# Kernel optimization log

Hardware: AMD Instinct MI355X
Metric: run time of the kernel (lower is better)

Reference implementation:

```python
import jax, jax.numpy as jnp
import numpy as np

D_MODEL = 512
HEADS = 8
CTX = 2048
BATCH = 4
SEQ = 2048


def make_rotary_matrix(context_window, d):
    # Faithful to the source, including theta = 10000 ** (-2*(i-1)/d)
    i = np.arange(d // 2)
    theta = 10000.0 ** (-2.0 * (i - 1) / d)  # [d/2]
    pos = np.arange(context_window)
    m_theta = pos[:, None] * theta[None, :]  # [m, d/2]
    cos, sin = np.cos(m_theta), np.sin(m_theta)
    R = np.zeros((context_window, d, d), dtype=np.float32)
    even, odd = 2 * i, 2 * i + 1
    R[:, even, even] = cos
    R[:, even, odd] = -sin
    R[:, odd, even] = sin
    R[:, odd, odd] = cos
    return jnp.asarray(R)


def setup_inputs() -> dict:
    key = jax.random.key(0)
    ks = jax.random.split(key, 8)
    s = 1.0 / np.sqrt(D_MODEL)
    x = jax.random.normal(ks[0], (BATCH, SEQ, D_MODEL), dtype=jnp.float32)
    Wq = jax.random.normal(ks[1], (D_MODEL, D_MODEL), dtype=jnp.float32) * s
    Wk = jax.random.normal(ks[2], (D_MODEL, D_MODEL), dtype=jnp.float32) * s
    Wv = jax.random.normal(ks[3], (D_MODEL, D_MODEL), dtype=jnp.float32) * s
    in_proj_w = jax.random.normal(ks[4], (3 * D_MODEL, D_MODEL), dtype=jnp.float32) * s
    in_proj_b = jax.random.normal(ks[5], (3 * D_MODEL,), dtype=jnp.float32) * 0.01
    out_w = jax.random.normal(ks[6], (D_MODEL, D_MODEL), dtype=jnp.float32) * s
    out_b = jax.random.normal(ks[7], (D_MODEL,), dtype=jnp.float32) * 0.01
    R = make_rotary_matrix(CTX, D_MODEL)
    return {"x": x, "Wq": Wq, "Wk": Wk, "Wv": Wv, "R": R,
            "in_proj_w": in_proj_w, "in_proj_b": in_proj_b,
            "out_w": out_w, "out_b": out_b}


def reference(x, Wq, Wk, Wv, R, in_proj_w, in_proj_b, out_w, out_b):
    b, m, d = x.shape
    h = HEADS
    hd = d // h
    # outer QKV projections (bias=False)
    q = x @ Wq.T
    k = x @ Wk.T
    v = x @ Wv.T
    # dense per-position rotary rotation: q_out[b,p,:] = q[b,p,:] @ R[p]
    Rm = R[:m]
    q = jnp.einsum('bmd,mde->bme', q, Rm)
    k = jnp.einsum('bmd,mde->bme', k, Rm)
    v = jnp.einsum('bmd,mde->bme', v, Rm)
    # nn.MultiheadAttention in_proj (bias=True) -- dropout skipped (eval)
    wq_i, wk_i, wv_i = jnp.split(in_proj_w, 3, axis=0)
    bq, bk, bv = jnp.split(in_proj_b, 3, axis=0)
    qp = (q @ wq_i.T + bq).reshape(b, m, h, hd).transpose(0, 2, 1, 3)
    kp = (k @ wk_i.T + bk).reshape(b, m, h, hd).transpose(0, 2, 1, 3)
    vp = (v @ wv_i.T + bv).reshape(b, m, h, hd).transpose(0, 2, 1, 3)
    scale = 1.0 / np.sqrt(hd)
    scores = jnp.einsum('bhqd,bhkd->bhqk', qp, kp) * scale
    causal = jnp.triu(jnp.full((m, m), -jnp.inf, dtype=scores.dtype), k=1)
    attn = jax.nn.softmax(scores + causal, axis=-1)
    out = jnp.einsum('bhqk,bhkd->bhqd', attn, vp)
    out = out.transpose(0, 2, 1, 3).reshape(b, m, d)
    return out @ out_w.T + out_b
```

## Files before the change

### kernel.cpp

```cpp
#include <hip/hip_runtime.h>
#include <cmath>

typedef unsigned short u16;
typedef __bf16 bf16x8 __attribute__((ext_vector_type(8)));
typedef float f32x4 __attribute__((ext_vector_type(4)));

#define SEQL 2048
#define NH 8
#define HD 64

static __device__ __forceinline__ u16 f2bf(float f) {
  union { float f; unsigned u; } v; v.f = f;
  unsigned u = v.u;
  unsigned r = (u + 0x7FFFu + ((u >> 16) & 1u)) >> 16;
  return (u16)r;
}
static __device__ __forceinline__ float bf2f(u16 h) {
  union { unsigned u; float f; } v; v.u = ((unsigned)h) << 16;
  return v.f;
}

__global__ __launch_bounds__(256) void cvt_kernel(const float* __restrict__ in,
                                                  u16* __restrict__ out, int n) {
  int i = (blockIdx.x * 256 + threadIdx.x) * 4;
  if (i < n) {
    float4 f = *(const float4*)(in + i);
    ushort4 o;
    o.x = f2bf(f.x); o.y = f2bf(f.y); o.z = f2bf(f.z); o.w = f2bf(f.w);
    *(ushort4*)(out + i) = o;
  }
}

__global__ __launch_bounds__(256) void rot_table_kernel(float2* __restrict__ T) {
  int m = blockIdx.x, i = threadIdx.x;
  double theta = pow(10000.0, -2.0 * ((double)i - 1.0) / 512.0);
  double a = (double)m * theta;
  T[m * 256 + i] = make_float2((float)cos(a), (float)sin(a));
}

__global__ __launch_bounds__(256) void rope_kernel(u16* __restrict__ QKV,
                                                   const float2* __restrict__ T) {
  int row = blockIdx.x;
  int i = threadIdx.x;
  int m = row & 2047;
  float2 cs = T[m * 256 + i];
  float c = cs.x, s = cs.y;
  size_t base = (size_t)row * 1536 + 2 * i;
  #pragma unroll
  for (int seg = 0; seg < 3; ++seg) {
    u16* p = QKV + base + seg * 512;
    ushort2 eo = *(ushort2*)p;
    float e = bf2f(eo.x), o = bf2f(eo.y);
    ushort2 w;
    w.x = f2bf(e * c + o * s);
    w.y = f2bf(-e * s + o * c);
    *(ushort2*)p = w;
  }
}

template<int MODE>
__global__ __launch_bounds__(256) void gemm_bt(const u16* __restrict__ A, int lda,
                                               const u16* __restrict__ B, int ldb,
                                               const float* __restrict__ bias,
                                               void* __restrict__ Cv, int ldc) {
  __shared__ u16 As[128 * 80];
  __shared__ u16 Bs[128 * 80];
  int tid = threadIdx.x;
  int wid = tid >> 6, lane = tid & 63, quad = lane >> 4, l16 = lane & 15;
  int m0 = blockIdx.y * 128, n0 = blockIdx.x * 128;
  int wm = (wid >> 1) * 64, wn = (wid & 1) * 64;
  f32x4 acc[4][4] = {};
  for (int kb = 0; kb < 512; kb += 64) {
    #pragma unroll
    for (int s = 0; s < 4; ++s) {
      int slot = tid + s * 256;
      int row = slot >> 3, seg = slot & 7;
      *(uint4*)(&As[row * 80 + seg * 8]) =
          *(const uint4*)(A + (size_t)(m0 + row) * lda + kb + seg * 8);
      *(uint4*)(&Bs[row * 80 + seg * 8]) =
          *(const uint4*)(B + (size_t)(n0 + row) * ldb + kb + seg * 8);
    }
    __syncthreads();
    #pragma unroll
    for (int kk = 0; kk < 2; ++kk) {
      bf16x8 af[4], bfr[4];
      #pragma unroll
      for (int i = 0; i < 4; ++i)
        af[i] = *(const bf16x8*)(&As[(wm + 16 * i + l16) * 80 + quad * 8 + kk * 32]);
      #pragma unroll
      for (int j = 0; j < 4; ++j)
        bfr[j] = *(const bf16x8*)(&Bs[(wn + 16 * j + l16) * 80 + quad * 8 + kk * 32]);
      #pragma unroll
      for (int i = 0; i < 4; ++i)
        #pragma unroll
        for (int j = 0; j < 4; ++j)
          acc[i][j] = __builtin_amdgcn_mfma_f32_16x16x32_bf16(af[i], bfr[j], acc[i][j], 0, 0, 0);
    }
    __syncthreads();
  }
  #pragma unroll
  for (int i = 0; i < 4; ++i)
    #pragma unroll
    for (int j = 0; j < 4; ++j)
      #pragma unroll
      for (int r = 0; r < 4; ++r) {
        int row = m0 + wm + 16 * i + quad * 4 + r;
        int col = n0 + wn + 16 * j + l16;
        float v = acc[i][j][r];
        if (MODE >= 1) v += bias[col];
        if (MODE == 0) {
          ((u16*)Cv)[(size_t)row * ldc + col] = f2bf(v);
        } else if (MODE == 1) {
          int bb = row >> 11, mm = row & 2047;
          int h = col >> 6, dd = col & 63;
          ((u16*)Cv)[(((size_t)(bb * NH + h)) * SEQL + mm) * HD + dd] = f2bf(v);
        } else {
          ((float*)Cv)[(size_t)row * ldc + col] = v;
        }
      }
}

__global__ __launch_bounds__(256) void flash_kernel(const u16* __restrict__ Q,
                                                    const u16* __restrict__ K,
                                                    const u16* __restrict__ V,
                                                    u16* __restrict__ O) {
  __shared__ u16 Ks[64 * 80];
  __shared__ u16 Vt[64 * 80];
  __shared__ u16 Ps[4 * 16 * 80];
  int tid = threadIdx.x;
  int wid = tid >> 6, lane = tid & 63, quad = lane >> 4, l16 = lane & 15;
  int bh = blockIdx.y;
  int b = bh >> 3, h = bh & 7;
  int q0 = blockIdx.x * 64;
  const u16* Qb = Q + (size_t)bh * SEQL * HD;
  const u16* Kb = K + (size_t)bh * SEQL * HD;
  const u16* Vb = V + (size_t)bh * SEQL * HD;

  int qrow = q0 + wid * 16 + l16;
  bf16x8 qfrag0 = *(const bf16x8*)(Qb + (size_t)qrow * HD + quad * 8);
  bf16x8 qfrag1 = *(const bf16x8*)(Qb + (size_t)qrow * HD + quad * 8 + 32);

  f32x4 o_acc[4] = {};
  float m_i[4], l_i[4];
  #pragma unroll
  for (int r = 0; r < 4; ++r) { m_i[r] = -__builtin_inff(); l_i[r] = 0.f; }

  int nkb = q0 / 64 + 1;
  for (int kb = 0; kb < nkb; ++kb) {
    int k0 = kb * 64;
    #pragma unroll
    for (int s = 0; s < 2; ++s) {
      int slot = tid + s * 256;
      int row = slot >> 3, seg = slot & 7;
      uint4 kv = *(const uint4*)(Kb + (size_t)(k0 + row) * HD + seg * 8);
      *(uint4*)(&Ks[row * 80 + seg * 8]) = kv;
      union { uint4 v; u16 hx[8]; } tv;
      tv.v = *(const uint4*)(Vb + (size_t)(k0 + row) * HD + seg * 8);
      #pragma unroll
      for (int e = 0; e < 8; ++e) Vt[(seg * 8 + e) * 80 + row] = tv.hx[e];
    }
    __syncthreads();

    f32x4 s_acc[4] = {};
    #pragma unroll
    for (int j = 0; j < 4; ++j) {
      bf16x8 bk0 = *(const bf16x8*)(&Ks[(j * 16 + l16) * 80 + quad * 8]);
      bf16x8 bk1 = *(const bf16x8*)(&Ks[(j * 16 + l16) * 80 + quad * 8 + 32]);
      s_acc[j] = __builtin_amdgcn_mfma_f32_16x16x32_bf16(qfrag0, bk0, s_acc[j], 0, 0, 0);
      s_acc[j] = __builtin_amdgcn_mfma_f32_16x16x32_bf16(qfrag1, bk1, s_acc[j], 0, 0, 0);
    }
    bool diag = (k0 == q0);
    #pragma unroll
    for (int j = 0; j < 4; ++j)
      #pragma unroll
      for (int r = 0; r < 4; ++r) {
        float sv = s_acc[j][r] * 0.125f;
        if (diag) {
          int keyl = j * 16 + l16;
          int rowl = wid * 16 + quad * 4 + r;
          if (keyl > rowl) sv = -__builtin_inff();
        }
        s_acc[j][r] = sv;
      }
    float p[4][4], alpha[4];
    #pragma unroll
    for (int r = 0; r < 4; ++r) {
      float mx = fmaxf(fmaxf(s_acc[0][r], s_acc[1][r]), fmaxf(s_acc[2][r], s_acc[3][r]));
      #pragma unroll
      for (int off = 1; off < 16; off <<= 1) mx = fmaxf(mx, __shfl_xor(mx, off, 64));
      float m_new = fmaxf(m_i[r], mx);
      alpha[r] = __expf(m_i[r] - m_new);
      float rs = 0.f;
      #pragma unroll
      for (int j = 0; j < 4; ++j) { float pv = __expf(s_acc[j][r] - m_new); p[j][r] = pv; rs += pv; }
      #pragma unroll
      for (int off = 1; off < 16; off <<= 1) rs += __shfl_xor(rs, off, 64);
      l_i[r] = l_i[r] * alpha[r] + rs;
      m_i[r] = m_new;
    }
    #pragma unroll
    for (int j = 0; j < 4; ++j)
      #pragma unroll
      for (int r = 0; r < 4; ++r) o_acc[j][r] *= alpha[r];

    u16* Pw = &Ps[wid * 16 * 80];
    #pragma unroll
    for (int j = 0; j < 4; ++j)
      #pragma unroll
      for (int r = 0; r < 4; ++r)
        Pw[(quad * 4 + r) * 80 + j * 16 + l16] = f2bf(p[j][r]);
    bf16x8 pf0 = *(const bf16x8*)(&Pw[l16 * 80 + quad * 8]);
    bf16x8 pf1 = *(const bf16x8*)(&Pw[l16 * 80 + quad * 8 + 32]);
    #pragma unroll
    for (int j = 0; j < 4; ++j) {
      bf16x8 bv0 = *(const bf16x8*)(&Vt[(j * 16 + l16) * 80 + quad * 8]);
      bf16x8 bv1 = *(const bf16x8*)(&Vt[(j * 16 + l16) * 80 + quad * 8 + 32]);
      o_acc[j] = __builtin_amdgcn_mfma_f32_16x16x32_bf16(pf0, bv0, o_acc[j], 0, 0, 0);
      o_acc[j] = __builtin_amdgcn_mfma_f32_16x16x32_bf16(pf1, bv1, o_acc[j], 0, 0, 0);
    }
    __syncthreads();
  }
  #pragma unroll
  for (int j = 0; j < 4; ++j)
    #pragma unroll
    for (int r = 0; r < 4; ++r) {
      int m = q0 + wid * 16 + quad * 4 + r;
      float v = o_acc[j][r] / l_i[r];
      O[((size_t)(b * SEQL + m)) * 512 + h * HD + j * 16 + l16] = f2bf(v);
    }
}

extern "C" void kernel_launch(void* const* d_in, const int* in_sizes, int n_in,
                              void* d_out, int out_size, void* d_ws, size_t ws_size,
                              hipStream_t stream) {
  const float* x   = (const float*)d_in[0];
  const float* Wq  = (const float*)d_in[1];
  const float* Wk  = (const float*)d_in[2];
  const float* Wv  = (const float*)d_in[3];
  const float* ipw = (const float*)d_in[5];
  const float* ipb = (const float*)d_in[6];
  const float* ow  = (const float*)d_in[7];
  const float* ob  = (const float*)d_in[8];
  float* out = (float*)d_out;

  char* w = (char*)d_ws;
  auto alloc = [&](size_t bytes) { void* p = w; w += bytes; return p; };
  u16* xb    = (u16*)alloc(8192UL * 512 * 2);
  u16* Wcatb = (u16*)alloc(3UL * 512 * 512 * 2);
  u16* ipwb  = (u16*)alloc(1536UL * 512 * 2);
  u16* owb   = (u16*)alloc(512UL * 512 * 2);
  u16* QKV0  = (u16*)alloc(8192UL * 1536 * 2);
  u16* qp    = (u16*)alloc(8192UL * 512 * 2);
  u16* kp    = (u16*)alloc(8192UL * 512 * 2);
  u16* vp    = (u16*)alloc(8192UL * 512 * 2);
  u16* Ob    = (u16*)alloc(8192UL * 512 * 2);
  float2* T  = (float2*)alloc(2048UL * 256 * sizeof(float2));

  rot_table_kernel<<<2048, 256, 0, stream>>>(T);
  cvt_kernel<<<4194304 / 1024, 256, 0, stream>>>(x, xb, 4194304);
  cvt_kernel<<<262144 / 1024, 256, 0, stream>>>(Wq, Wcatb, 262144);
  cvt_kernel<<<262144 / 1024, 256, 0, stream>>>(Wk, Wcatb + 262144, 262144);
  cvt_kernel<<<262144 / 1024, 256, 0, stream>>>(Wv, Wcatb + 524288, 262144);
  cvt_kernel<<<786432 / 1024, 256, 0, stream>>>(ipw, ipwb, 786432);
  cvt_kernel<<<262144 / 1024, 256, 0, stream>>>(ow, owb, 262144);

  gemm_bt<0><<<dim3(12, 64), 256, 0, stream>>>(xb, 512, Wcatb, 512, nullptr, QKV0, 1536);
  rope_kernel<<<8192, 256, 0, stream>>>(QKV0, T);
  gemm_bt<1><<<dim3(4, 64), 256, 0, stream>>>(QKV0,        1536, ipwb,               512, ipb,        qp, 0);
  gemm_bt<1><<<dim3(4, 64), 256, 0, stream>>>(QKV0 + 512,  1536, ipwb + 512 * 512,   512, ipb + 512,  kp, 0);
  gemm_bt<1><<<dim3(4, 64), 256, 0, stream>>>(QKV0 + 1024, 1536, ipwb + 1024 * 512,  512, ipb + 1024, vp, 0);
  flash_kernel<<<dim3(32, 32), 256, 0, stream>>>(qp, kp, vp, Ob);
  gemm_bt<2><<<dim3(4, 64), 256, 0, stream>>>(Ob, 512, owb, 512, ob, out, 512);
}
```

Measured before the change: 2.531 ms.

## Merge in-proj GEMMs, pre-transpose V, and give each flash block two query tiles

The three per-segment in-projection GEMMs become one launch, which writes Q and K in head-major layout and V already transposed. The flash kernel now loads V tiles with vector copies instead of scalar LDS scatter-transposes. Each flash block processes 128 query rows as two 64-row tiles that share every K/V tile load, halving K/V traffic per query. The cost is fewer blocks (512), more registers per thread, and strided scalar stores for the transposed V in the GEMM epilogue.

```diff
diff --git a/kernel.cpp b/kernel.cpp
--- a/kernel.cpp
+++ b/kernel.cpp
@@ -8,6 +8,7 @@
 #define SEQL 2048
 #define NH 8
 #define HD 64
+#define MROWS 8192
 
 static __device__ __forceinline__ u16 f2bf(float f) {
   union { float f; unsigned u; } v; v.f = f;
@@ -74,11 +75,11 @@
     #pragma unroll
     for (int s = 0; s < 4; ++s) {
       int slot = tid + s * 256;
-      int row = slot >> 3, seg = slot & 7;
-      *(uint4*)(&As[row * 80 + seg * 8]) =
-          *(const uint4*)(A + (size_t)(m0 + row) * lda + kb + seg * 8);
-      *(uint4*)(&Bs[row * 80 + seg * 8]) =
-          *(const uint4*)(B + (size_t)(n0 + row) * ldb + kb + seg * 8);
+      int row = slot >> 3, sg = slot & 7;
+      *(uint4*)(&As[row * 80 + sg * 8]) =
+          *(const uint4*)(A + (size_t)(m0 + row) * lda + kb + sg * 8);
+      *(uint4*)(&Bs[row * 80 + sg * 8]) =
+          *(const uint4*)(B + (size_t)(n0 + row) * ldb + kb + sg * 8);
     }
     __syncthreads();
     #pragma unroll
@@ -107,22 +108,140 @@
         int row = m0 + wm + 16 * i + quad * 4 + r;
         int col = n0 + wn + 16 * j + l16;
         float v = acc[i][j][r];
-        if (MODE >= 1) v += bias[col];
+        if (MODE == 2) v += bias[col];
         if (MODE == 0) {
           ((u16*)Cv)[(size_t)row * ldc + col] = f2bf(v);
-        } else if (MODE == 1) {
-          int bb = row >> 11, mm = row & 2047;
-          int h = col >> 6, dd = col & 63;
-          ((u16*)Cv)[(((size_t)(bb * NH + h)) * SEQL + mm) * HD + dd] = f2bf(v);
         } else {
           ((float*)Cv)[(size_t)row * ldc + col] = v;
         }
       }
 }
 
+__global__ __launch_bounds__(256) void gemm_inproj(const u16* __restrict__ Aall,
+                                                   const u16* __restrict__ B,
+                                                   const float* __restrict__ bias,
+                                                   u16* __restrict__ qkvh) {
+  __shared__ u16 As[128 * 80];
+  __shared__ u16 Bs[128 * 80];
+  int tid = threadIdx.x;
+  int wid = tid >> 6, lane = tid & 63, quad = lane >> 4, l16 = lane & 15;
+  int m0 = blockIdx.y * 128, n0 = blockIdx.x * 128;
+  int qseg = n0 >> 9;
+  const u16* A = Aall + qseg * 512;
+  int wm = (wid >> 1) * 64, wn = (wid & 1) * 64;
+  f32x4 acc[4][4] = {};
+  for (int kb = 0; kb < 512; kb += 64) {
+    #pragma unroll
+    for (int s = 0; s < 4; ++s) {
+      int slot = tid + s * 256;
+      int row = slot >> 3, sg = slot & 7;
+      *(uint4*)(&As[row * 80 + sg * 8]) =
+          *(const uint4*)(A + (size_t)(m0 + row) * 1536 + kb + sg * 8);
+      *(uint4*)(&Bs[row * 80 + sg * 8]) =
+          *(const uint4*)(B + (size_t)(n0 + row) * 512 + kb + sg * 8);
+    }
+    __syncthreads();
+    #pragma unroll
+    for (int kk = 0; kk < 2; ++kk) {
+      bf16x8 af[4], bfr[4];
+      #pragma unroll
+      for (int i = 0; i < 4; ++i)
+        af[i] = *(const bf16x8*)(&As[(wm + 16 * i + l16) * 80 + quad * 8 + kk * 32]);
+      #pragma unroll
+      for (int j = 0; j < 4; ++j)
+        bfr[j] = *(const bf16x8*)(&Bs[(wn + 16 * j + l16) * 80 + quad * 8 + kk * 32]);
+      #pragma unroll
+      for (int i = 0; i < 4; ++i)
+        #pragma unroll
+        for (int j = 0; j < 4; ++j)
+          acc[i][j] = __builtin_amdgcn_mfma_f32_16x16x32_bf16(af[i], bfr[j], acc[i][j], 0, 0, 0);
+    }
+    __syncthreads();
+  }
+  #pragma unroll
+  for (int i = 0; i < 4; ++i)
+    #pragma unroll
+    for (int j = 0; j < 4; ++j)
+      #pragma unroll
+      for (int r = 0; r < 4; ++r) {
+        int row = m0 + wm + 16 * i + quad * 4 + r;
+        int col = n0 + wn + 16 * j + l16;
+        float v = acc[i][j][r] + bias[col];
+        int cl = col & 511;
+        int h = cl >> 6, dd = cl & 63;
+        int bb = row >> 11, mm = row & 2047;
+        if (qseg < 2) {
+          qkvh[(size_t)qseg * MROWS * 512 +
+               (((size_t)(bb * NH + h)) * SEQL + mm) * HD + dd] = f2bf(v);
+        } else {
+          qkvh[(size_t)2 * MROWS * 512 +
+               ((size_t)(bb * NH + h) * HD + dd) * SEQL + mm] = f2bf(v);
+        }
+      }
+}
+
+static __device__ __forceinline__ f32x4 mfma_bf16(bf16x8 a, bf16x8 b, f32x4 c) {
+  return __builtin_amdgcn_mfma_f32_16x16x32_bf16(a, b, c, 0, 0, 0);
+}
+
+static __device__ __forceinline__ void attn_tile(
+    bf16x8 qf0, bf16x8 qf1, f32x4* o_acc, float* m_i, float* l_i,
+    const u16* Ks, const u16* Vt, u16* Pw, bool diag, int wrow, int quad, int l16) {
+  f32x4 s_acc[4] = {};
+  #pragma unroll
+  for (int j = 0; j < 4; ++j) {
+    bf16x8 bk0 = *(const bf16x8*)(&Ks[(j * 16 + l16) * 80 + quad * 8]);
+    bf16x8 bk1 = *(const bf16x8*)(&Ks[(j * 16 + l16) * 80 + quad * 8 + 32]);
+    s_acc[j] = mfma_bf16(qf0, bk0, s_acc[j]);
+    s_acc[j] = mfma_bf16(qf1, bk1, s_acc[j]);
+  }
+  #pragma unroll
+  for (int j = 0; j < 4; ++j)
+    #pragma unroll
+    for (int r = 0; r < 4; ++r) {
+      float sv = s_acc[j][r] * 0.125f;
+      if (diag && (j * 16 + l16 > wrow + quad * 4 + r)) sv = -__builtin_inff();
+      s_acc[j][r] = sv;
+    }
+  float p[4][4], alpha[4];
+  #pragma unroll
+  for (int r = 0; r < 4; ++r) {
+    float mx = fmaxf(fmaxf(s_acc[0][r], s_acc[1][r]), fmaxf(s_acc[2][r], s_acc[3][r]));
+    #pragma unroll
+    for (int off = 1; off < 16; off <<= 1) mx = fmaxf(mx, __shfl_xor(mx, off, 64));
+    float m_new = fmaxf(m_i[r], mx);
+    alpha[r] = __expf(m_i[r] - m_new);
+    float rs = 0.f;
+    #pragma unroll
+    for (int j = 0; j < 4; ++j) { float pv = __expf(s_acc[j][r] - m_new); p[j][r] = pv; rs += pv; }
+    #pragma unroll
+    for (int off = 1; off < 16; off <<= 1) rs += __shfl_xor(rs, off, 64);
+    l_i[r] = l_i[r] * alpha[r] + rs;
+    m_i[r] = m_new;
+  }
+  #pragma unroll
+  for (int j = 0; j < 4; ++j)
+    #pragma unroll
+    for (int r = 0; r < 4; ++r) o_acc[j][r] *= alpha[r];
+  #pragma unroll
+  for (int j = 0; j < 4; ++j)
+    #pragma unroll
+    for (int r = 0; r < 4; ++r)
+      Pw[(quad * 4 + r) * 80 + j * 16 + l16] = f2bf(p[j][r]);
+  bf16x8 pf0 = *(const bf16x8*)(&Pw[l16 * 80 + quad * 8]);
+  bf16x8 pf1 = *(const bf16x8*)(&Pw[l16 * 80 + quad * 8 + 32]);
+  #pragma unroll
+  for (int j = 0; j < 4; ++j) {
+    bf16x8 bv0 = *(const bf16x8*)(&Vt[(j * 16 + l16) * 80 + quad * 8]);
+    bf16x8 bv1 = *(const bf16x8*)(&Vt[(j * 16 + l16) * 80 + quad * 8 + 32]);
+    o_acc[j] = mfma_bf16(pf0, bv0, o_acc[j]);
+    o_acc[j] = mfma_bf16(pf1, bv1, o_acc[j]);
+  }
+}
+
 __global__ __launch_bounds__(256) void flash_kernel(const u16* __restrict__ Q,
                                                     const u16* __restrict__ K,
-                                                    const u16* __restrict__ V,
+                                                    const u16* __restrict__ Vt_g,
                                                     u16* __restrict__ O) {
   __shared__ u16 Ks[64 * 80];
   __shared__ u16 Vt[64 * 80];
@@ -131,102 +250,53 @@
   int wid = tid >> 6, lane = tid & 63, quad = lane >> 4, l16 = lane & 15;
   int bh = blockIdx.y;
   int b = bh >> 3, h = bh & 7;
-  int q0 = blockIdx.x * 64;
+  int q0 = blockIdx.x * 128;
   const u16* Qb = Q + (size_t)bh * SEQL * HD;
   const u16* Kb = K + (size_t)bh * SEQL * HD;
-  const u16* Vb = V + (size_t)bh * SEQL * HD;
-
-  int qrow = q0 + wid * 16 + l16;
-  bf16x8 qfrag0 = *(const bf16x8*)(Qb + (size_t)qrow * HD + quad * 8);
-  bf16x8 qfrag1 = *(const bf16x8*)(Qb + (size_t)qrow * HD + quad * 8 + 32);
-
-  f32x4 o_acc[4] = {};
-  float m_i[4], l_i[4];
-  #pragma unroll
-  for (int r = 0; r < 4; ++r) { m_i[r] = -__builtin_inff(); l_i[r] = 0.f; }
-
-  int nkb = q0 / 64 + 1;
+  const u16* Vb = Vt_g + (size_t)bh * HD * SEQL;
+  u16* Pw = &Ps[wid * 16 * 80];
+
+  int rowA = q0 + wid * 16 + l16;
+  int rowB = rowA + 64;
+  bf16x8 qA0 = *(const bf16x8*)(Qb + (size_t)rowA * HD + quad * 8);
+  bf16x8 qA1 = *(const bf16x8*)(Qb + (size_t)rowA * HD + quad * 8 + 32);
+  bf16x8 qB0 = *(const bf16x8*)(Qb + (size_t)rowB * HD + quad * 8);
+  bf16x8 qB1 = *(const bf16x8*)(Qb + (size_t)rowB * HD + quad * 8 + 32);
+
+  f32x4 oA[4] = {}, oB[4] = {};
+  float mA[4], lA[4], mB[4], lB[4];
+  #pragma unroll
+  for (int r = 0; r < 4; ++r) {
+    mA[r] = -__builtin_inff(); lA[r] = 0.f;
+    mB[r] = -__builtin_inff(); lB[r] = 0.f;
+  }
+
+  int nkb = q0 / 64 + 2;
   for (int kb = 0; kb < nkb; ++kb) {
     int k0 = kb * 64;
     #pragma unroll
     for (int s = 0; s < 2; ++s) {
       int slot = tid + s * 256;
-      int row = slot >> 3, seg = slot & 7;
-      uint4 kv = *(const uint4*)(Kb + (size_t)(k0 + row) * HD + seg * 8);
-      *(uint4*)(&Ks[row * 80 + seg * 8]) = kv;
-      union { uint4 v; u16 hx[8]; } tv;
-      tv.v = *(const uint4*)(Vb + (size_t)(k0 + row) * HD + seg * 8);
-      #pragma unroll
-      for (int e = 0; e < 8; ++e) Vt[(seg * 8 + e) * 80 + row] = tv.hx[e];
-    }
-    __syncthreads();
-
-    f32x4 s_acc[4] = {};
-    #pragma unroll
-    for (int j = 0; j < 4; ++j) {
-      bf16x8 bk0 = *(const bf16x8*)(&Ks[(j * 16 + l16) * 80 + quad * 8]);
-      bf16x8 bk1 = *(const bf16x8*)(&Ks[(j * 16 + l16) * 80 + quad * 8 + 32]);
-      s_acc[j] = __builtin_amdgcn_mfma_f32_16x16x32_bf16(qfrag0, bk0, s_acc[j], 0, 0, 0);
-      s_acc[j] = __builtin_amdgcn_mfma_f32_16x16x32_bf16(qfrag1, bk1, s_acc[j], 0, 0, 0);
-    }
-    bool diag = (k0 == q0);
-    #pragma unroll
-    for (int j = 0; j < 4; ++j)
-      #pragma unroll
-      for (int r = 0; r < 4; ++r) {
-        float sv = s_acc[j][r] * 0.125f;
-        if (diag) {
-          int keyl = j * 16 + l16;
-          int rowl = wid * 16 + quad * 4 + r;
-          if (keyl > rowl) sv = -__builtin_inff();
-        }
-        s_acc[j][r] = sv;
-      }
-    float p[4][4], alpha[4];
+      int row = slot >> 3, sg = slot & 7;
+      *(uint4*)(&Ks[row * 80 + sg * 8]) =
+          *(const uint4*)(Kb + (size_t)(k0 + row) * HD + sg * 8);
+      *(uint4*)(&Vt[row * 80 + sg * 8]) =
+          *(const uint4*)(Vb + (size_t)row * SEQL + k0 + sg * 8);
+    }
+    __syncthreads();
+    if (kb < nkb - 1)
+      attn_tile(qA0, qA1, oA, mA, lA, Ks, Vt, Pw, kb == nkb - 2, wid * 16, quad, l16);
+    attn_tile(qB0, qB1, oB, mB, lB, Ks, Vt, Pw, kb == nkb - 1, wid * 16, quad, l16);
+    __syncthreads();
+  }
+  #pragma unroll
+  for (int j = 0; j < 4; ++j)
     #pragma unroll
     for (int r = 0; r < 4; ++r) {
-      float mx = fmaxf(fmaxf(s_acc[0][r], s_acc[1][r]), fmaxf(s_acc[2][r], s_acc[3][r]));
-      #pragma unroll
-      for (int off = 1; off < 16; off <<= 1) mx = fmaxf(mx, __shfl_xor(mx, off, 64));
-      float m_new = fmaxf(m_i[r], mx);
-      alpha[r] = __expf(m_i[r] - m_new);
-      float rs = 0.f;
-      #pragma unroll
-      for (int j = 0; j < 4; ++j) { float pv = __expf(s_acc[j][r] - m_new); p[j][r] = pv; rs += pv; }
-      #pragma unroll
-      for (int off = 1; off < 16; off <<= 1) rs += __shfl_xor(rs, off, 64);
-      l_i[r] = l_i[r] * alpha[r] + rs;
-      m_i[r] = m_new;
-    }
-    #pragma unroll
-    for (int j = 0; j < 4; ++j)
-      #pragma unroll
-      for (int r = 0; r < 4; ++r) o_acc[j][r] *= alpha[r];
-
-    u16* Pw = &Ps[wid * 16 * 80];
-    #pragma unroll
-    for (int j = 0; j < 4; ++j)
-      #pragma unroll
-      for (int r = 0; r < 4; ++r)
-        Pw[(quad * 4 + r) * 80 + j * 16 + l16] = f2bf(p[j][r]);
-    bf16x8 pf0 = *(const bf16x8*)(&Pw[l16 * 80 + quad * 8]);
-    bf16x8 pf1 = *(const bf16x8*)(&Pw[l16 * 80 + quad * 8 + 32]);
-    #pragma unroll
-    for (int j = 0; j < 4; ++j) {
-      bf16x8 bv0 = *(const bf16x8*)(&Vt[(j * 16 + l16) * 80 + quad * 8]);
-      bf16x8 bv1 = *(const bf16x8*)(&Vt[(j * 16 + l16) * 80 + quad * 8 + 32]);
-      o_acc[j] = __builtin_amdgcn_mfma_f32_16x16x32_bf16(pf0, bv0, o_acc[j], 0, 0, 0);
-      o_acc[j] = __builtin_amdgcn_mfma_f32_16x16x32_bf16(pf1, bv1, o_acc[j], 0, 0, 0);
-    }
-    __syncthreads();
-  }
-  #pragma unroll
-  for (int j = 0; j < 4; ++j)
-    #pragma unroll
-    for (int r = 0; r < 4; ++r) {
-      int m = q0 + wid * 16 + quad * 4 + r;
-      float v = o_acc[j][r] / l_i[r];
-      O[((size_t)(b * SEQL + m)) * 512 + h * HD + j * 16 + l16] = f2bf(v);
+      int mA_idx = q0 + wid * 16 + quad * 4 + r;
+      O[((size_t)(b * SEQL + mA_idx)) * 512 + h * HD + j * 16 + l16] = f2bf(oA[j][r] / lA[r]);
+      int mB_idx = mA_idx + 64;
+      O[((size_t)(b * SEQL + mB_idx)) * 512 + h * HD + j * 16 + l16] = f2bf(oB[j][r] / lB[r]);
     }
 }
 
@@ -250,9 +320,7 @@
   u16* ipwb  = (u16*)alloc(1536UL * 512 * 2);
   u16* owb   = (u16*)alloc(512UL * 512 * 2);
   u16* QKV0  = (u16*)alloc(8192UL * 1536 * 2);
-  u16* qp    = (u16*)alloc(8192UL * 512 * 2);
-  u16* kp    = (u16*)alloc(8192UL * 512 * 2);
-  u16* vp    = (u16*)alloc(8192UL * 512 * 2);
+  u16* qkvh  = (u16*)alloc(3UL * 8192 * 512 * 2);
   u16* Ob    = (u16*)alloc(8192UL * 512 * 2);
   float2* T  = (float2*)alloc(2048UL * 256 * sizeof(float2));
 
@@ -266,9 +334,8 @@
 
   gemm_bt<0><<<dim3(12, 64), 256, 0, stream>>>(xb, 512, Wcatb, 512, nullptr, QKV0, 1536);
   rope_kernel<<<8192, 256, 0, stream>>>(QKV0, T);
-  gemm_bt<1><<<dim3(4, 64), 256, 0, stream>>>(QKV0,        1536, ipwb,               512, ipb,        qp, 0);
-  gemm_bt<1><<<dim3(4, 64), 256, 0, stream>>>(QKV0 + 512,  1536, ipwb + 512 * 512,   512, ipb + 512,  kp, 0);
-  gemm_bt<1><<<dim3(4, 64), 256, 0, stream>>>(QKV0 + 1024, 1536, ipwb + 1024 * 512,  512, ipb + 1024, vp, 0);
-  flash_kernel<<<dim3(32, 32), 256, 0, stream>>>(qp, kp, vp, Ob);
+  gemm_inproj<<<dim3(12, 64), 256, 0, stream>>>(QKV0, ipwb, ipb, qkvh);
+  flash_kernel<<<dim3(16, 32), 256, 0, stream>>>(
+      qkvh, qkvh + 8192UL * 512, qkvh + 2UL * 8192 * 512, Ob);
   gemm_bt<2><<<dim3(4, 64), 256, 0, stream>>>(Ob, 512, owb, 512, ob, out, 512);
 }
```

After: 2.577 ms. Within noise of the previous version (+1.8%).
